# Optimization experiments

Measured on AMD Instinct MI355X. Metric: run time of the kernel, lower is better.

## Reference

```python
import jax, jax.numpy as jnp
import numpy as np

D_WIN = 6
SIGMA = D_WIN / 2.0  # sigma = D/2
EPS = 1e-6


def _ln(x, g, b):
    m = jnp.mean(x, -1, keepdims=True)
    v = jnp.var(x, -1, keepdims=True)
    return (x - m) / jnp.sqrt(v + EPS) * g + b


def _cross_attn(q, kv, Wq, Wkv, Wproj, bproj, nh):
    # standard multi-head cross attention, no qkv bias (qkv_bias=False)
    B, S, C = q.shape
    N = kv.shape[1]
    hd = C // nh
    scale = hd ** -0.5
    qh = (q @ Wq).reshape(B, S, nh, hd).transpose(0, 2, 1, 3) * scale
    kvh = (kv @ Wkv).reshape(B, N, 2, nh, hd).transpose(2, 0, 3, 1, 4)
    k, v = kvh[0], kvh[1]
    attn = jax.nn.softmax(jnp.einsum('bhsd,bhnd->bhsn', qh, k), -1)
    x = jnp.einsum('bhsn,bhnd->bhsd', attn, v).transpose(0, 2, 1, 3).reshape(B, S, C)
    return x @ Wproj + bproj


def setup_inputs() -> dict:
    key = jax.random.key(0)
    ks = jax.random.split(key, 32)
    B, S, C, H, W = 32, 128, 384, 8, 512

    def lin(k, i, o):
        return jax.random.normal(k, (i, o), jnp.float32) * 0.02

    inp = {
        'q': jax.random.normal(ks[0], (B, S, C), jnp.float32),
        'kv': jax.random.normal(ks[1], (B, H * W, C), jnp.float32),
        # main attention linears (qkv_bias=False)
        'Wq': lin(ks[2], C, C),
        'Wkv': lin(ks[3], C, 2 * C),
        'Wproj': lin(ks[4], C, C), 'bproj': jnp.zeros((C,), jnp.float32),
        # position predictor
        'Wp_w': lin(ks[5], C, C), 'Wp_b': jnp.zeros((C,), jnp.float32),
        'vp_w': lin(ks[6], C, 1), 'vp_b': jnp.zeros((1,), jnp.float32),
        'Wqpos': lin(ks[7], C, C), 'bqpos': jnp.zeros((C,), jnp.float32),
        # simplified RCTC decoder projection
        'Wrctc': lin(ks[8], C, C), 'brctc': jnp.zeros((C,), jnp.float32),
        # pt_to_question cross attention (2 heads)
        'ca1_Wq': lin(ks[9], C, C), 'ca1_Wkv': lin(ks[10], C, 2 * C),
        'ca1_Wproj': lin(ks[11], C, C), 'ca1_bproj': jnp.zeros((C,), jnp.float32),
        # pt_to_image cross attention (2 heads)
        'ca2_Wq': lin(ks[12], C, C), 'ca2_Wkv': lin(ks[13], C, 2 * C),
        'ca2_Wproj': lin(ks[14], C, C), 'ca2_bproj': jnp.zeros((C,), jnp.float32),
        # layernorms
        'g_q1': jnp.ones((C,), jnp.float32), 'b_q1': jnp.zeros((C,), jnp.float32),
        'g_kv1': jnp.ones((C,), jnp.float32), 'b_kv1': jnp.zeros((C,), jnp.float32),
        'g_q2': jnp.ones((C,), jnp.float32), 'b_q2': jnp.zeros((C,), jnp.float32),
        'g_kv2': jnp.ones((C,), jnp.float32), 'b_kv2': jnp.zeros((C,), jnp.float32),
        'sz_h': H, 'sz_w': W,
    }
    return inp


def reference(q, kv, Wq, Wkv, Wproj, bproj, Wp_w, Wp_b, vp_w, vp_b, Wqpos, bqpos,
              Wrctc, brctc, ca1_Wq, ca1_Wkv, ca1_Wproj, ca1_bproj,
              ca2_Wq, ca2_Wkv, ca2_Wproj, ca2_bproj,
              g_q1, b_q1, g_kv1, b_kv1, g_q2, b_q2, g_kv2, b_kv2, sz_h, sz_w):
    B, N, C = kv.shape
    S = q.shape[1]
    H, W = sz_h, sz_w
    nh = 1
    hd = C // nh
    scale = hd ** -0.5

    # RCTC decoder (simplified): (B,N,C) -> (B,C,H,W) -> collapse H -> (B,W,C) -> linear
    kv_img = kv.transpose(0, 2, 1).reshape(B, C, H, W)
    dec = kv_img.mean(axis=2).transpose(0, 2, 1)  # (B, W, C)
    dec = dec @ Wrctc + brctc

    qh = (q @ Wq).reshape(B, S, nh, hd).transpose(0, 2, 1, 3) * scale  # (B,nh,S,hd)
    kvh = (dec @ Wkv).reshape(B, W, 2, nh, hd).transpose(2, 0, 3, 1, 4)
    k, v = kvh[0], kvh[1]  # (B,nh,W,hd)

    # position prediction branch
    p = q @ Wqpos + bqpos
    p = _cross_attn(_ln(p, g_q1, b_q1), _ln(q, g_kv1, b_kv1),
                    ca1_Wq, ca1_Wkv, ca1_Wproj, ca1_bproj, 2)
    p = _cross_attn(_ln(p, g_q2, b_q2), _ln(dec, g_kv2, b_kv2),
                    ca2_Wq, ca2_Wkv, ca2_Wproj, ca2_bproj, 2)
    p_t = jax.nn.sigmoid(jnp.tanh(p @ Wp_w + Wp_b) @ vp_w + vp_b) * W  # (B,S,1)

    # Gaussian window mask around predicted position
    idx = jnp.arange(W, dtype=jnp.float32)[None, None, None, :]     # (1,1,1,W)
    pexp = p_t[:, None, :, :]                                        # (B,1,S,1)
    gauss = jnp.exp(-(idx - pexp) ** 2 / (2.0 * SIGMA ** 2))         # (B,1,S,W)

    attn = jnp.einsum('bhsd,bhwd->bhsw', qh, k) * gauss
    attn = jax.nn.softmax(attn, -1)
    x = jnp.einsum('bhsw,bhwd->bhsd', attn, v).transpose(0, 2, 1, 3).reshape(B, S, C)
    return x @ Wproj + bproj
```

## Files before the change

### kernel.cpp

```cpp
#include <hip/hip_runtime.h>
#include <hip/hip_bf16.h>
#include <math.h>

#define B_ 32
#define S_ 128
#define C_ 384
#define H_ 8
#define W_ 512
#define NKV 4096

typedef __attribute__((ext_vector_type(8))) short short8;
typedef __attribute__((ext_vector_type(4))) float floatx4;

static __device__ __forceinline__ ushort f2bf(float v) {
    __hip_bfloat16 h = __float2bfloat16(v);
    return *(ushort*)&h;
}
static __device__ __forceinline__ float ldf(const float* p, size_t i) { return p[i]; }
static __device__ __forceinline__ float ldf(const ushort* p, size_t i) {
    union { uint u; float f; } c; c.u = (uint)p[i] << 16; return c.f;
}

__global__ __launch_bounds__(256) void prep_kernel(const float* __restrict__ kv,
                                                   ushort* __restrict__ dec0b,
                                                   const float* __restrict__ q,
                                                   ushort* __restrict__ qb) {
    int v = blockIdx.x * 256 + threadIdx.x;
    const int meanTot = B_ * W_ * (C_ / 4);
    if (v < meanTot) {
        int c4  = v % (C_ / 4);
        int row = v / (C_ / 4);
        int b = row / W_;
        int w = row % W_;
        const float4* src = (const float4*)kv + (size_t)(b * NKV + w) * (C_ / 4) + c4;
        float4 s = {0.f, 0.f, 0.f, 0.f};
#pragma unroll
        for (int h = 0; h < H_; ++h) {
            float4 t = src[(size_t)h * W_ * (C_ / 4)];
            s.x += t.x; s.y += t.y; s.z += t.z; s.w += t.w;
        }
        ushort4 o;
        o.x = f2bf(s.x * 0.125f); o.y = f2bf(s.y * 0.125f);
        o.z = f2bf(s.z * 0.125f); o.w = f2bf(s.w * 0.125f);
        ((ushort4*)dec0b)[v] = o;
        return;
    }
    v -= meanTot;
    const int castTot = B_ * S_ * (C_ / 4);
    if (v >= castTot) return;
    float4 f = ((const float4*)q)[v];
    ushort4 o;
    o.x = f2bf(f.x); o.y = f2bf(f.y); o.z = f2bf(f.z); o.w = f2bf(f.w);
    ((ushort4*)qb)[v] = o;
}

struct WtDesc { const float* src[12]; ushort* dst[12]; int Kd[12]; int Nd[12]; };
__global__ __launch_bounds__(256) void wtcast_kernel(WtDesc d) {
    int wi = blockIdx.y;
    int K = d.Kd[wi], N = d.Nd[wi];
    int tiles_n = N / 32;
    int tile = blockIdx.x;
    if (tile >= (K / 32) * tiles_n) return;
    int k0 = (tile / tiles_n) * 32, n0 = (tile % tiles_n) * 32;
    __shared__ float t[32][33];
    int tid = threadIdx.x;
    int r = tid >> 3, c4 = (tid & 7) * 4;
    float4 v = *(const float4*)&d.src[wi][(size_t)(k0 + r) * N + n0 + c4];
    t[r][c4] = v.x; t[r][c4 + 1] = v.y; t[r][c4 + 2] = v.z; t[r][c4 + 3] = v.w;
    __syncthreads();
    int c = tid >> 3, k4 = (tid & 7) * 4;
    ushort4 o;
    o.x = f2bf(t[k4][c]); o.y = f2bf(t[k4 + 1][c]);
    o.z = f2bf(t[k4 + 2][c]); o.w = f2bf(t[k4 + 3][c]);
    *(ushort4*)&d.dst[wi][(size_t)(n0 + c) * K + k0 + k4] = o;
}

struct GJob {
    const ushort* A; const ushort* Bt;
    const float* bias; float* Cout; ushort* Cbf;
    int M, N, K; float alpha; int act;
};
struct GJobs { GJob j[3]; };

__global__ __launch_bounds__(256) void bgemm_kernel(GJobs gs) {
    const GJob g = gs.j[blockIdx.z];
    const int bm = blockIdx.y * 128, bn = blockIdx.x * 128;
    if (bm >= g.M || bn >= g.N) return;
    __shared__ ushort As[128 * 40];
    __shared__ ushort Bs[128 * 40];
    const int tid = threadIdx.x;
    const int wav = tid >> 6, lane = tid & 63;
    const int wm = (wav >> 1) * 64, wn = (wav & 1) * 64;
    const int lrow = lane & 15, lq = lane >> 4;

    floatx4 acc[4][4] = {};

    const int sr = tid >> 1, sc0 = (tid & 1) * 16;
    const ushort* Ag = g.A + (size_t)(bm + sr) * g.K + sc0;
    const ushort* Bg = g.Bt + (size_t)(bn + sr) * g.K + sc0;
    ushort* Asw = &As[sr * 40 + sc0];
    ushort* Bsw = &Bs[sr * 40 + sc0];

    uint4 a0 = *(const uint4*)(Ag);
    uint4 a1 = *(const uint4*)(Ag + 8);
    uint4 b0 = *(const uint4*)(Bg);
    uint4 b1 = *(const uint4*)(Bg + 8);

    for (int k0 = 0; k0 < g.K; k0 += 32) {
        __syncthreads();
        *(uint4*)Asw = a0; *(uint4*)(Asw + 8) = a1;
        *(uint4*)Bsw = b0; *(uint4*)(Bsw + 8) = b1;
        __syncthreads();
        if (k0 + 32 < g.K) {
            a0 = *(const uint4*)(Ag + k0 + 32);
            a1 = *(const uint4*)(Ag + k0 + 40);
            b0 = *(const uint4*)(Bg + k0 + 32);
            b1 = *(const uint4*)(Bg + k0 + 40);
        }
        short8 af[4], bfr[4];
#pragma unroll
        for (int i = 0; i < 4; ++i)
            af[i] = *(const short8*)&As[(wm + 16 * i + lrow) * 40 + lq * 8];
#pragma unroll
        for (int j = 0; j < 4; ++j)
            bfr[j] = *(const short8*)&Bs[(wn + 16 * j + lrow) * 40 + lq * 8];
#pragma unroll
        for (int i = 0; i < 4; ++i)
#pragma unroll
            for (int j = 0; j < 4; ++j)
                acc[i][j] = __builtin_amdgcn_mfma_f32_16x16x32_bf16(af[i], bfr[j], acc[i][j], 0, 0, 0);
    }

#pragma unroll
    for (int i = 0; i < 4; ++i)
#pragma unroll
        for (int j = 0; j < 4; ++j) {
            int row = bm + wm + 16 * i + lq * 4;
            int col = bn + wn + 16 * j + lrow;
            float bv = g.bias ? g.bias[col] : 0.f;
#pragma unroll
            for (int r = 0; r < 4; ++r) {
                float v = acc[i][j][r] * g.alpha + bv;
                if (g.act == 1) v = tanhf(v);
                size_t off = (size_t)(row + r) * g.N + col;
                if (g.Cout) g.Cout[off] = v;
                if (g.Cbf) g.Cbf[off] = f2bf(v);
            }
        }
}

static inline void bgemmJ(hipStream_t st, int nj, const GJob* js) {
    GJobs gs;
    int mx = 0, my = 0;
    for (int i = 0; i < nj; ++i) {
        gs.j[i] = js[i];
        int nx = js[i].N / 128, ny = js[i].M / 128;
        if (nx > mx) mx = nx;
        if (ny > my) my = ny;
    }
    for (int i = nj; i < 3; ++i) gs.j[i] = js[0];
    bgemm_kernel<<<dim3(mx, my, nj), 256, 0, st>>>(gs);
}

struct BGArgs {
    const ushort* A; const ushort* Bt;
    const float* bias; float* outF; ushort* outB;
    int lda, ldb, ldo;
    long AsB, BsB, OsB;
    int AsH, BsH, OsH;
    int K, NH;
    float alpha; int act;
    int nbat;
    const ushort* vtsrc; ushort* vtdst; int vtNw;
};
__global__ __launch_bounds__(256) void battn_kernel(BGArgs g) {
    __shared__ ushort As[64 * 40];
    __shared__ ushort Bs[64 * 40];
    const int tid = threadIdx.x;
    const int bat = blockIdx.z;
    if (bat >= g.nbat) {
        int flat = (bat - g.nbat) * (gridDim.x * gridDim.y)
                 + blockIdx.y * gridDim.x + blockIdx.x;
        int wt_n = g.vtNw >> 5;
        int tiles = wt_n * (C_ / 32);
        if (flat >= B_ * tiles) return;
        int b  = flat / tiles, rr = flat % tiles;
        int w0 = (rr % wt_n) * 32, c0 = (rr / wt_n) * 32;
        ushort (*t)[33] = (ushort (*)[33])As;
        int wl = tid >> 3, c4 = (tid & 7) * 4;
        ushort4 v = *(const ushort4*)&g.vtsrc[((size_t)b * g.vtNw + w0 + wl) * 768 + 384 + c0 + c4];
        t[wl][c4] = v.x; t[wl][c4 + 1] = v.y; t[wl][c4 + 2] = v.z; t[wl][c4 + 3] = v.w;
        __syncthreads();
        int dl = tid >> 3, w4 = (tid & 7) * 4;
        ushort4 o;
        o.x = t[w4][dl]; o.y = t[w4 + 1][dl]; o.z = t[w4 + 2][dl]; o.w = t[w4 + 3][dl];
        *(ushort4*)&g.vtdst[((size_t)b * C_ + c0 + dl) * g.vtNw + w0 + w4] = o;
        return;
    }
    const int bn = blockIdx.x * 64, bm = blockIdx.y * 64;
    const int bb = bat / g.NH, hh = bat % g.NH;
    const ushort* A  = g.A  + (size_t)bb * g.AsB + (size_t)hh * g.AsH;
    const ushort* Bt = g.Bt + (size_t)bb * g.BsB + (size_t)hh * g.BsH;
    const int wav = tid >> 6, lane = tid & 63;
    const int lrow = lane & 15, lq = lane >> 4;
    const int sr = tid >> 2, sc0 = (tid & 3) * 8;
    const ushort* Ag = A  + (size_t)(bm + sr) * g.lda + sc0;
    const ushort* Bg = Bt + (size_t)(bn + sr) * g.ldb + sc0;
    ushort* Asw = &As[sr * 40 + sc0];
    ushort* Bsw = &Bs[sr * 40 + sc0];

    floatx4 acc[4] = {};

    uint4 a = *(const uint4*)(Ag);
    uint4 b = *(const uint4*)(Bg);

    for (int k0 = 0; k0 < g.K; k0 += 32) {
        __syncthreads();
        *(uint4*)Asw = a; *(uint4*)Bsw = b;
        __syncthreads();
        if (k0 + 32 < g.K) {
            a = *(const uint4*)(Ag + k0 + 32);
            b = *(const uint4*)(Bg + k0 + 32);
        }
        short8 af = *(const short8*)&As[(wav * 16 + lrow) * 40 + lq * 8];
#pragma unroll
        for (int j = 0; j < 4; ++j) {
            short8 bf = *(const short8*)&Bs[(16 * j + lrow) * 40 + lq * 8];
            acc[j] = __builtin_amdgcn_mfma_f32_16x16x32_bf16(af, bf, acc[j], 0, 0, 0);
        }
    }

#pragma unroll
    for (int j = 0; j < 4; ++j) {
        int col = bn + 16 * j + lrow;
        float bv = g.bias ? g.bias[col] : 0.f;
        int row0 = bm + wav * 16 + lq * 4;
#pragma unroll
        for (int r = 0; r < 4; ++r) {
            float v = acc[j][r] * g.alpha + bv;
            if (g.act == 1) v = tanhf(v);
            size_t off = (size_t)bb * g.OsB + (size_t)hh * g.OsH
                       + (size_t)(row0 + r) * g.ldo + col;
            if (g.outF) g.outF[off] = v;
            if (g.outB) g.outB[off] = f2bf(v);
        }
    }
}

static inline void battn(hipStream_t st, const ushort* A, const ushort* Bt,
                         const float* bias, float* outF, ushort* outB,
                         int M, int N, int K, float alpha, int act,
                         int lda, long AsB, int AsH,
                         int ldb, long BsB, int BsH,
                         int ldo, long OsB, int OsH,
                         int NH, int nbat,
                         const ushort* vtsrc = nullptr, ushort* vtdst = nullptr,
                         int vtNw = 0) {
    BGArgs g;
    g.A = A; g.Bt = Bt; g.bias = bias; g.outF = outF; g.outB = outB;
    g.lda = lda; g.ldb = ldb; g.ldo = ldo;
    g.AsB = AsB; g.BsB = BsB; g.OsB = OsB;
    g.AsH = AsH; g.BsH = BsH; g.OsH = OsH;
    g.K = K; g.NH = NH; g.alpha = alpha; g.act = act;
    g.nbat = nbat; g.vtsrc = vtsrc; g.vtdst = vtdst; g.vtNw = vtNw;
    int gx = N / 64, gy = M / 64, gz = nbat;
    if (vtsrc) {
        int nvt = B_ * (vtNw / 32) * (C_ / 32);
        int per = gx * gy;
        gz += (nvt + per - 1) / per;
    }
    battn_kernel<<<dim3(gx, gy, gz), 256, 0, st>>>(g);
}

static inline void bgemm64(hipStream_t st, const ushort* A, const ushort* Bt,
                           const float* bias, float* outF, ushort* outB,
                           int M, int N, int K, float alpha, int act) {
    battn(st, A, Bt, bias, outF, outB, M, N, K, alpha, act,
          K, 0, 0, K, 0, 0, N, 0, 0, 1, 1);
}

struct Ln2Desc {
    const void* X0; const float* g0; const float* b0; ushort* Y0; int bf0; int rows0;
    const void* X1; const float* g1; const float* b1; ushort* Y1; int bf1;
};
__global__ __launch_bounds__(128) void ln2_kernel(Ln2Desc d) {
    int row = blockIdx.x;
    const void* X; const float* g; const float* bb; ushort* Y; int isbf;
    if (row < d.rows0) { X = d.X0; g = d.g0; bb = d.b0; Y = d.Y0; isbf = d.bf0; }
    else { row -= d.rows0; X = d.X1; g = d.g1; bb = d.b1; Y = d.Y1; isbf = d.bf1; }
    const float*  xf = (const float*)X + (size_t)row * C_;
    const ushort* xb = (const ushort*)X + (size_t)row * C_;
    ushort* y = Y + (size_t)row * C_;
    int t = threadIdx.x;
    float v0, v1, v2;
    if (isbf) { v0 = ldf(xb, t); v1 = ldf(xb, t + 128); v2 = ldf(xb, t + 256); }
    else      { v0 = ldf(xf, t); v1 = ldf(xf, t + 128); v2 = ldf(xf, t + 256); }
    float s = v0 + v1 + v2, sq = v0 * v0 + v1 * v1 + v2 * v2;
    __shared__ float rs[128], rq[128];
    rs[t] = s; rq[t] = sq; __syncthreads();
    if (t < 64) {
        s = rs[t] + rs[t + 64]; sq = rq[t] + rq[t + 64];
        for (int o = 32; o; o >>= 1) { s += __shfl_down(s, o); sq += __shfl_down(sq, o); }
        if (t == 0) { rs[0] = s; rq[0] = sq; }
    }
    __syncthreads();
    float mean = rs[0] * (1.0f / C_);
    float var  = rq[0] * (1.0f / C_) - mean * mean;
    float inv  = rsqrtf(var + 1e-6f);
    y[t]       = f2bf((v0 - mean) * inv * g[t]       + bb[t]);
    y[t + 128] = f2bf((v1 - mean) * inv * g[t + 128] + bb[t + 128]);
    y[t + 256] = f2bf((v2 - mean) * inv * g[t + 256] + bb[t + 256]);
}

template <int NW, int GAUSS>
__global__ __launch_bounds__(256) void softmax_kernel(
    const float* __restrict__ sc, const float* __restrict__ ptv,
    ushort* __restrict__ P)
{
    int row = blockIdx.x * 4 + (threadIdx.x >> 6);
    int lane = threadIdx.x & 63;
    const float* s = sc + (size_t)row * NW;
    float pcen = GAUSS ? ptv[row] : 0.f;
    float vals[NW / 64];
    float m = -1e30f;
#pragma unroll
    for (int i = 0; i < NW / 64; ++i) {
        int w = lane + 64 * i;
        float v = s[w];
        if (GAUSS) { float dw = (float)w - pcen; v *= expf(dw * dw * (-1.0f / 18.0f)); }
        vals[i] = v; m = fmaxf(m, v);
    }
#pragma unroll
    for (int o = 32; o; o >>= 1) m = fmaxf(m, __shfl_xor(m, o));
    float sum = 0.f;
#pragma unroll
    for (int i = 0; i < NW / 64; ++i) { vals[i] = expf(vals[i] - m); sum += vals[i]; }
#pragma unroll
    for (int o = 32; o; o >>= 1) sum += __shfl_xor(sum, o);
    float rinv = 1.0f / sum;
    ushort* op = P + (size_t)row * NW;
#pragma unroll
    for (int i = 0; i < NW / 64; ++i) op[lane + 64 * i] = f2bf(vals[i] * rinv);
}

__global__ __launch_bounds__(128) void pt_kernel(const float* __restrict__ T,
    const float* __restrict__ vpw, const float* __restrict__ vpb,
    float* __restrict__ out) {
    int row = blockIdx.x;
    int t = threadIdx.x;
    const float* x = T + (size_t)row * C_;
    float s = x[t] * vpw[t] + x[t + 128] * vpw[t + 128] + x[t + 256] * vpw[t + 256];
    __shared__ float red[128];
    red[t] = s; __syncthreads();
    if (t < 64) {
        s = red[t] + red[t + 64];
        for (int o = 32; o; o >>= 1) s += __shfl_down(s, o);
        if (t == 0) {
            float z = s + vpb[0];
            out[row] = 512.0f / (1.0f + expf(-z));
        }
    }
}

extern "C" void kernel_launch(void* const* d_in, const int* in_sizes, int n_in,
                              void* d_out, int out_size, void* d_ws, size_t ws_size,
                              hipStream_t stream) {
    const float* q     = (const float*)d_in[0];
    const float* kv    = (const float*)d_in[1];
    const float* Wq    = (const float*)d_in[2];
    const float* Wkv   = (const float*)d_in[3];
    const float* Wproj = (const float*)d_in[4];
    const float* bproj = (const float*)d_in[5];
    const float* Wp_w  = (const float*)d_in[6];
    const float* Wp_b  = (const float*)d_in[7];
    const float* vp_w  = (const float*)d_in[8];
    const float* vp_b  = (const float*)d_in[9];
    const float* Wqpos = (const float*)d_in[10];
    const float* bqpos = (const float*)d_in[11];
    const float* Wrctc = (const float*)d_in[12];
    const float* brctc = (const float*)d_in[13];
    const float* ca1_Wq    = (const float*)d_in[14];
    const float* ca1_Wkv   = (const float*)d_in[15];
    const float* ca1_Wproj = (const float*)d_in[16];
    const float* ca1_bproj = (const float*)d_in[17];
    const float* ca2_Wq    = (const float*)d_in[18];
    const float* ca2_Wkv   = (const float*)d_in[19];
    const float* ca2_Wproj = (const float*)d_in[20];
    const float* ca2_bproj = (const float*)d_in[21];
    const float* g_q1  = (const float*)d_in[22];
    const float* b_q1  = (const float*)d_in[23];
    const float* g_kv1 = (const float*)d_in[24];
    const float* b_kv1 = (const float*)d_in[25];
    const float* g_q2  = (const float*)d_in[26];
    const float* b_q2  = (const float*)d_in[27];
    const float* g_kv2 = (const float*)d_in[28];
    const float* b_kv2 = (const float*)d_in[29];
    float* out = (float*)d_out;
    float* ws  = (float*)d_ws;

    ushort* dec0b = (ushort*)(ws);
    ushort* wb    = (ushort*)(ws + 3145728);
    ushort* qb    = (ushort*)(ws + 4251648);
    ushort* decb  = (ushort*)(ws + 5038080);
    ushort* qhb   = (ushort*)(ws + 8183808);
    float*  p     = ws + 8970240;
    ushort* pb    = (ushort*)(ws + 10543104);
    float*  t1    = ws + 11329536;
    ushort* t1b   = (ushort*)(ws + 12902400);
    ushort* t2b   = (ushort*)(ws + 13688832);
    ushort* qpb   = (ushort*)(ws + 16834560);
    ushort* kvb   = (ushort*)(ws + 17620992);
    ushort* vt    = (ushort*)(ws + 23912448);
    float*  sc    = ws + 27058176;
    ushort* Pb    = (ushort*)(ws + 31252480);
    ushort* xb    = (ushort*)(ws + 33349632);
    float*  ptb   = ws + 34136064;

    ushort* wbWq     = wb;
    ushort* wbWqpos  = wb + 147456;
    ushort* wbWrctc  = wb + 294912;
    ushort* wbC1Wq   = wb + 442368;
    ushort* wbC1Wp   = wb + 589824;
    ushort* wbC2Wq   = wb + 737280;
    ushort* wbC2Wp   = wb + 884736;
    ushort* wbWpw    = wb + 1032192;
    ushort* wbWproj  = wb + 1179648;
    ushort* wbWkv    = wb + 1327104;
    ushort* wbC1Wkv  = wb + 1622016;
    ushort* wbC2Wkv  = wb + 1916928;

    const float rs384 = 0.05103103630798288f;
    const float rs192 = 0.07216878364870323f;

    prep_kernel<<<(B_ * W_ * (C_ / 4) + B_ * S_ * (C_ / 4) + 255) / 256, 256, 0, stream>>>(
        kv, dec0b, q, qb);
    {
        WtDesc d;
        const float* s_[12] = {Wq, Wqpos, Wrctc, ca1_Wq, ca1_Wproj, ca2_Wq, ca2_Wproj,
                               Wp_w, Wproj, Wkv, ca1_Wkv, ca2_Wkv};
        ushort* t_[12] = {wbWq, wbWqpos, wbWrctc, wbC1Wq, wbC1Wp, wbC2Wq, wbC2Wp,
                          wbWpw, wbWproj, wbWkv, wbC1Wkv, wbC2Wkv};
        for (int i = 0; i < 12; ++i) {
            d.src[i] = s_[i]; d.dst[i] = t_[i];
            d.Kd[i] = 384; d.Nd[i] = (i >= 9) ? 768 : 384;
        }
        dim3 grid(288, 12);
        wtcast_kernel<<<grid, 256, 0, stream>>>(d);
    }
    {
        GJob js[3];
        js[0] = {dec0b, wbWrctc, brctc, nullptr, decb, B_ * W_, 384, 384, 1.f, 0};
        js[1] = {qb, wbWq, nullptr, nullptr, qhb, B_ * S_, 384, 384, rs384, 0};
        js[2] = {qb, wbWqpos, bqpos, p, nullptr, B_ * S_, 384, 384, 1.f, 0};
        bgemmJ(stream, 3, js);
    }
    {
        Ln2Desc d;
        d.X0 = p; d.g0 = g_q1;  d.b0 = b_q1;  d.Y0 = t1b; d.bf0 = 0; d.rows0 = B_ * S_;
        d.X1 = q; d.g1 = g_kv1; d.b1 = b_kv1; d.Y1 = t2b; d.bf1 = 0;
        ln2_kernel<<<2 * B_ * S_, 128, 0, stream>>>(d);
    }
    {
        GJob js[2];
        js[0] = {t1b, wbC1Wq, nullptr, nullptr, qpb, B_ * S_, 384, 384, rs192, 0};
        js[1] = {t2b, wbC1Wkv, nullptr, nullptr, kvb, B_ * S_, 768, 384, 1.f, 0};
        bgemmJ(stream, 2, js);
    }
    battn(stream, qpb, kvb, nullptr, sc, nullptr, 128, 128, 192, 1.f, 0,
          384, (long)S_ * 384, 192,
          768, (long)S_ * 768, 192,
          128, (long)2 * S_ * 128, S_ * 128, 2, 64,
          kvb, vt, S_);
    softmax_kernel<128, 0><<<(B_ * 2 * S_) / 4, 256, 0, stream>>>(sc, nullptr, Pb);
    battn(stream, Pb, vt, nullptr, nullptr, xb, 128, 192, 128, 1.f, 0,
          128, (long)2 * S_ * 128, S_ * 128,
          128, (long)C_ * S_, 192 * S_,
          384, (long)S_ * 384, 192, 2, 64);
    bgemm64(stream, xb, wbC1Wp, ca1_bproj, p, nullptr, B_ * S_, 384, 384, 1.f, 0);
    {
        Ln2Desc d;
        d.X0 = p;    d.g0 = g_q2;  d.b0 = b_q2;  d.Y0 = t1b; d.bf0 = 0; d.rows0 = B_ * S_;
        d.X1 = decb; d.g1 = g_kv2; d.b1 = b_kv2; d.Y1 = t2b; d.bf1 = 1;
        ln2_kernel<<<B_ * S_ + B_ * W_, 128, 0, stream>>>(d);
    }
    {
        GJob js[2];
        js[0] = {t1b, wbC2Wq, nullptr, nullptr, qpb, B_ * S_, 384, 384, rs192, 0};
        js[1] = {t2b, wbC2Wkv, nullptr, nullptr, kvb, B_ * W_, 768, 384, 1.f, 0};
        bgemmJ(stream, 2, js);
    }
    battn(stream, qpb, kvb, nullptr, sc, nullptr, 128, 512, 192, 1.f, 0,
          384, (long)S_ * 384, 192,
          768, (long)W_ * 768, 192,
          512, (long)2 * S_ * 512, S_ * 512, 2, 64,
          kvb, vt, W_);
    softmax_kernel<512, 0><<<(B_ * 2 * S_) / 4, 256, 0, stream>>>(sc, nullptr, Pb);
    battn(stream, Pb, vt, nullptr, nullptr, xb, 128, 192, 512, 1.f, 0,
          512, (long)2 * S_ * 512, S_ * 512,
          512, (long)C_ * W_, 192 * W_,
          384, (long)S_ * 384, 192, 2, 64);
    bgemm64(stream, xb, wbC2Wp, ca2_bproj, p, pb, B_ * S_, 384, 384, 1.f, 0);
    {
        GJob js[2];
        js[0] = {pb, wbWpw, Wp_b, t1, nullptr, B_ * S_, 384, 384, 1.f, 1};
        js[1] = {decb, wbWkv, nullptr, nullptr, kvb, B_ * W_, 768, 384, 1.f, 0};
        bgemmJ(stream, 2, js);
    }
    pt_kernel<<<B_ * S_, 128, 0, stream>>>(t1, vp_w, vp_b, ptb);
    battn(stream, qhb, kvb, nullptr, sc, nullptr, 128, 512, 384, 1.f, 0,
          384, (long)S_ * 384, 0,
          768, (long)W_ * 768, 0,
          512, (long)S_ * 512, 0, 1, 32,
          kvb, vt, W_);
    softmax_kernel<512, 1><<<(B_ * S_) / 4, 256, 0, stream>>>(sc, ptb, Pb);
    battn(stream, Pb, vt, nullptr, nullptr, xb, 128, 384, 512, 1.f, 0,
          512, (long)S_ * 512, 0,
          512, (long)C_ * W_, 0,
          384, (long)S_ * 384, 0, 1, 32);
    bgemm64(stream, xb, wbWproj, bproj, out, nullptr, B_ * S_, 384, 384, 1.f, 0);
}
```

Measured before the change: 562.4 us.

## Fuse softmax into PV matmul and merge prep/weight-cast kernels

Replaces the separate softmax kernels and the following P·V batched GEMMs with one kernel. It computes each row's max and sum from the fp32 scores, then rebuilds the bf16 probabilities tile by tile while doing the MFMA product, scaling by the reciprocal sum at the end. This removes the bf16 P round-trip through global memory and three kernel launches. The input prep and weight-cast kernels are also merged into one launch. In exchange, each output-column block recomputes the row statistics and exponentials, which reads the score matrix several times and adds redundant expf work.

```diff
diff --git a/kernel.cpp b/kernel.cpp
--- a/kernel.cpp
+++ b/kernel.cpp
@@ -21,58 +21,58 @@
     union { uint u; float f; } c; c.u = (uint)p[i] << 16; return c.f;
 }
 
-__global__ __launch_bounds__(256) void prep_kernel(const float* __restrict__ kv,
-                                                   ushort* __restrict__ dec0b,
-                                                   const float* __restrict__ q,
-                                                   ushort* __restrict__ qb) {
-    int v = blockIdx.x * 256 + threadIdx.x;
-    const int meanTot = B_ * W_ * (C_ / 4);
-    if (v < meanTot) {
+struct PrepDesc {
+    const float* kv; ushort* dec0b; const float* q; ushort* qb;
+    const float* wsrc[12]; ushort* wdst[12]; int wN[12];
+};
+__global__ __launch_bounds__(256) void prep2_kernel(PrepDesc d) {
+    __shared__ float t[32][33];
+    const int meanB = B_ * W_ * (C_ / 4) / 256;
+    const int castB = B_ * S_ * (C_ / 4) / 256;
+    int bid = blockIdx.x;
+    int tid = threadIdx.x;
+    if (bid < meanB) {
+        int v = bid * 256 + tid;
         int c4  = v % (C_ / 4);
         int row = v / (C_ / 4);
         int b = row / W_;
         int w = row % W_;
-        const float4* src = (const float4*)kv + (size_t)(b * NKV + w) * (C_ / 4) + c4;
+        const float4* src = (const float4*)d.kv + (size_t)(b * NKV + w) * (C_ / 4) + c4;
         float4 s = {0.f, 0.f, 0.f, 0.f};
 #pragma unroll
         for (int h = 0; h < H_; ++h) {
-            float4 t = src[(size_t)h * W_ * (C_ / 4)];
-            s.x += t.x; s.y += t.y; s.z += t.z; s.w += t.w;
+            float4 x = src[(size_t)h * W_ * (C_ / 4)];
+            s.x += x.x; s.y += x.y; s.z += x.z; s.w += x.w;
         }
         ushort4 o;
         o.x = f2bf(s.x * 0.125f); o.y = f2bf(s.y * 0.125f);
         o.z = f2bf(s.z * 0.125f); o.w = f2bf(s.w * 0.125f);
-        ((ushort4*)dec0b)[v] = o;
+        ((ushort4*)d.dec0b)[v] = o;
         return;
     }
-    v -= meanTot;
-    const int castTot = B_ * S_ * (C_ / 4);
-    if (v >= castTot) return;
-    float4 f = ((const float4*)q)[v];
-    ushort4 o;
-    o.x = f2bf(f.x); o.y = f2bf(f.y); o.z = f2bf(f.z); o.w = f2bf(f.w);
-    ((ushort4*)qb)[v] = o;
-}
-
-struct WtDesc { const float* src[12]; ushort* dst[12]; int Kd[12]; int Nd[12]; };
-__global__ __launch_bounds__(256) void wtcast_kernel(WtDesc d) {
-    int wi = blockIdx.y;
-    int K = d.Kd[wi], N = d.Nd[wi];
+    if (bid < meanB + castB) {
+        int v = (bid - meanB) * 256 + tid;
+        float4 f = ((const float4*)d.q)[v];
+        ushort4 o;
+        o.x = f2bf(f.x); o.y = f2bf(f.y); o.z = f2bf(f.z); o.w = f2bf(f.w);
+        ((ushort4*)d.qb)[v] = o;
+        return;
+    }
+    int f = bid - meanB - castB;
+    int wi = f / 288, tile = f % 288;
+    int N = d.wN[wi];
     int tiles_n = N / 32;
-    int tile = blockIdx.x;
-    if (tile >= (K / 32) * tiles_n) return;
+    if (tile >= 12 * tiles_n) return;
     int k0 = (tile / tiles_n) * 32, n0 = (tile % tiles_n) * 32;
-    __shared__ float t[32][33];
-    int tid = threadIdx.x;
     int r = tid >> 3, c4 = (tid & 7) * 4;
-    float4 v = *(const float4*)&d.src[wi][(size_t)(k0 + r) * N + n0 + c4];
+    float4 v = *(const float4*)&d.wsrc[wi][(size_t)(k0 + r) * N + n0 + c4];
     t[r][c4] = v.x; t[r][c4 + 1] = v.y; t[r][c4 + 2] = v.z; t[r][c4 + 3] = v.w;
     __syncthreads();
     int c = tid >> 3, k4 = (tid & 7) * 4;
     ushort4 o;
     o.x = f2bf(t[k4][c]); o.y = f2bf(t[k4 + 1][c]);
     o.z = f2bf(t[k4 + 2][c]); o.w = f2bf(t[k4 + 3][c]);
-    *(ushort4*)&d.dst[wi][(size_t)(n0 + c) * K + k0 + k4] = o;
+    *(ushort4*)&d.wdst[wi][(size_t)(n0 + c) * 384 + k0 + k4] = o;
 }
 
 struct GJob {
@@ -279,6 +279,103 @@
           K, 0, 0, K, 0, 0, N, 0, 0, 1, 1);
 }
 
+struct PVArgs {
+    const float* sc; const float* ptv; const ushort* Bt; ushort* outB;
+    int ldb, ldo; long BsB, OsB; int BsH, OsH; int NH;
+};
+template <int NW, int GAUSS>
+__global__ __launch_bounds__(256) void pvsm_kernel(PVArgs g) {
+    __shared__ ushort As[64 * 40];
+    __shared__ ushort Bs[64 * 40];
+    __shared__ float msh[64], rsh[64];
+    const int bn = blockIdx.x * 64, bm = blockIdx.y * 64;
+    const int bat = blockIdx.z, bb = bat / g.NH, hh = bat % g.NH;
+    const int tid = threadIdx.x;
+    const int wav = tid >> 6, lane = tid & 63;
+    const int lrow = lane & 15, lq = lane >> 4;
+    const float* Sg = g.sc + (size_t)bat * S_ * NW + (size_t)bm * NW;
+
+    for (int rr = wav * 16; rr < wav * 16 + 16; ++rr) {
+        float pcen = 0.f;
+        if (GAUSS) pcen = g.ptv[(size_t)bat * S_ + bm + rr];
+        float v[NW / 64];
+        float m = -1e30f;
+#pragma unroll
+        for (int i = 0; i < NW / 64; ++i) {
+            int w = lane + 64 * i;
+            float x = Sg[(size_t)rr * NW + w];
+            if (GAUSS) { float dw = (float)w - pcen; x *= expf(dw * dw * (-1.0f / 18.0f)); }
+            v[i] = x; m = fmaxf(m, x);
+        }
+#pragma unroll
+        for (int o = 32; o; o >>= 1) m = fmaxf(m, __shfl_xor(m, o));
+        float s = 0.f;
+#pragma unroll
+        for (int i = 0; i < NW / 64; ++i) s += expf(v[i] - m);
+#pragma unroll
+        for (int o = 32; o; o >>= 1) s += __shfl_xor(s, o);
+        if (lane == 0) { msh[rr] = m; rsh[rr] = 1.0f / s; }
+    }
+    __syncthreads();
+
+    const int sr = tid >> 2, sc0 = (tid & 3) * 8;
+    const ushort* Bg = g.Bt + (size_t)bb * g.BsB + (size_t)hh * g.BsH
+                     + (size_t)(bn + sr) * g.ldb + sc0;
+    ushort* Asw = &As[sr * 40 + sc0];
+    ushort* Bsw = &Bs[sr * 40 + sc0];
+    const float mrow = msh[sr];
+    float pcen_s = 0.f;
+    if (GAUSS) pcen_s = g.ptv[(size_t)bat * S_ + bm + sr];
+    const float* Ssr = Sg + (size_t)sr * NW;
+
+    floatx4 acc[4] = {};
+    float4 f0 = *(const float4*)(Ssr + sc0);
+    float4 f1 = *(const float4*)(Ssr + sc0 + 4);
+    uint4 b = *(const uint4*)(Bg);
+
+    for (int k0 = 0; k0 < NW; k0 += 32) {
+        float xv[8] = {f0.x, f0.y, f0.z, f0.w, f1.x, f1.y, f1.z, f1.w};
+        ushort av[8] __attribute__((aligned(16)));
+#pragma unroll
+        for (int j = 0; j < 8; ++j) {
+            float x = xv[j];
+            if (GAUSS) {
+                float dw = (float)(k0 + sc0 + j) - pcen_s;
+                x *= expf(dw * dw * (-1.0f / 18.0f));
+            }
+            av[j] = f2bf(expf(x - mrow));
+        }
+        __syncthreads();
+        *(uint4*)Asw = *(const uint4*)av;
+        *(uint4*)Bsw = b;
+        __syncthreads();
+        if (k0 + 32 < NW) {
+            f0 = *(const float4*)(Ssr + k0 + 32 + sc0);
+            f1 = *(const float4*)(Ssr + k0 + 36 + sc0);
+            b  = *(const uint4*)(Bg + k0 + 32);
+        }
+        short8 af = *(const short8*)&As[(wav * 16 + lrow) * 40 + lq * 8];
+#pragma unroll
+        for (int j = 0; j < 4; ++j) {
+            short8 bf = *(const short8*)&Bs[(16 * j + lrow) * 40 + lq * 8];
+            acc[j] = __builtin_amdgcn_mfma_f32_16x16x32_bf16(af, bf, acc[j], 0, 0, 0);
+        }
+    }
+
+#pragma unroll
+    for (int j = 0; j < 4; ++j) {
+        int col = bn + 16 * j + lrow;
+        int lr0 = wav * 16 + lq * 4;
+#pragma unroll
+        for (int r = 0; r < 4; ++r) {
+            float v = acc[j][r] * rsh[lr0 + r];
+            size_t off = (size_t)bb * g.OsB + (size_t)hh * g.OsH
+                       + (size_t)(bm + lr0 + r) * g.ldo + col;
+            g.outB[off] = f2bf(v);
+        }
+    }
+}
+
 struct Ln2Desc {
     const void* X0; const float* g0; const float* b0; ushort* Y0; int bf0; int rows0;
     const void* X1; const float* g1; const float* b1; ushort* Y1; int bf1;
@@ -310,37 +407,6 @@
     y[t]       = f2bf((v0 - mean) * inv * g[t]       + bb[t]);
     y[t + 128] = f2bf((v1 - mean) * inv * g[t + 128] + bb[t + 128]);
     y[t + 256] = f2bf((v2 - mean) * inv * g[t + 256] + bb[t + 256]);
-}
-
-template <int NW, int GAUSS>
-__global__ __launch_bounds__(256) void softmax_kernel(
-    const float* __restrict__ sc, const float* __restrict__ ptv,
-    ushort* __restrict__ P)
-{
-    int row = blockIdx.x * 4 + (threadIdx.x >> 6);
-    int lane = threadIdx.x & 63;
-    const float* s = sc + (size_t)row * NW;
-    float pcen = GAUSS ? ptv[row] : 0.f;
-    float vals[NW / 64];
-    float m = -1e30f;
-#pragma unroll
-    for (int i = 0; i < NW / 64; ++i) {
-        int w = lane + 64 * i;
-        float v = s[w];
-        if (GAUSS) { float dw = (float)w - pcen; v *= expf(dw * dw * (-1.0f / 18.0f)); }
-        vals[i] = v; m = fmaxf(m, v);
-    }
-#pragma unroll
-    for (int o = 32; o; o >>= 1) m = fmaxf(m, __shfl_xor(m, o));
-    float sum = 0.f;
-#pragma unroll
-    for (int i = 0; i < NW / 64; ++i) { vals[i] = expf(vals[i] - m); sum += vals[i]; }
-#pragma unroll
-    for (int o = 32; o; o >>= 1) sum += __shfl_xor(sum, o);
-    float rinv = 1.0f / sum;
-    ushort* op = P + (size_t)row * NW;
-#pragma unroll
-    for (int i = 0; i < NW / 64; ++i) op[lane + 64 * i] = f2bf(vals[i] * rinv);
 }
 
 __global__ __launch_bounds__(128) void pt_kernel(const float* __restrict__ T,
@@ -412,7 +478,6 @@
     ushort* kvb   = (ushort*)(ws + 17620992);
     ushort* vt    = (ushort*)(ws + 23912448);
     float*  sc    = ws + 27058176;
-    ushort* Pb    = (ushort*)(ws + 31252480);
     ushort* xb    = (ushort*)(ws + 33349632);
     float*  ptb   = ws + 34136064;
 
@@ -432,20 +497,18 @@
     const float rs384 = 0.05103103630798288f;
     const float rs192 = 0.07216878364870323f;
 
-    prep_kernel<<<(B_ * W_ * (C_ / 4) + B_ * S_ * (C_ / 4) + 255) / 256, 256, 0, stream>>>(
-        kv, dec0b, q, qb);
-    {
-        WtDesc d;
+    {
+        PrepDesc d;
+        d.kv = kv; d.dec0b = dec0b; d.q = q; d.qb = qb;
         const float* s_[12] = {Wq, Wqpos, Wrctc, ca1_Wq, ca1_Wproj, ca2_Wq, ca2_Wproj,
                                Wp_w, Wproj, Wkv, ca1_Wkv, ca2_Wkv};
         ushort* t_[12] = {wbWq, wbWqpos, wbWrctc, wbC1Wq, wbC1Wp, wbC2Wq, wbC2Wp,
                           wbWpw, wbWproj, wbWkv, wbC1Wkv, wbC2Wkv};
         for (int i = 0; i < 12; ++i) {
-            d.src[i] = s_[i]; d.dst[i] = t_[i];
-            d.Kd[i] = 384; d.Nd[i] = (i >= 9) ? 768 : 384;
-        }
-        dim3 grid(288, 12);
-        wtcast_kernel<<<grid, 256, 0, stream>>>(d);
+            d.wsrc[i] = s_[i]; d.wdst[i] = t_[i];
+            d.wN[i] = (i >= 9) ? 768 : 384;
+        }
+        prep2_kernel<<<6144 + 1536 + 3456, 256, 0, stream>>>(d);
     }
     {
         GJob js[3];
@@ -471,11 +534,14 @@
           768, (long)S_ * 768, 192,
           128, (long)2 * S_ * 128, S_ * 128, 2, 64,
           kvb, vt, S_);
-    softmax_kernel<128, 0><<<(B_ * 2 * S_) / 4, 256, 0, stream>>>(sc, nullptr, Pb);
-    battn(stream, Pb, vt, nullptr, nullptr, xb, 128, 192, 128, 1.f, 0,
-          128, (long)2 * S_ * 128, S_ * 128,
-          128, (long)C_ * S_, 192 * S_,
-          384, (long)S_ * 384, 192, 2, 64);
+    {
+        PVArgs a;
+        a.sc = sc; a.ptv = nullptr; a.Bt = vt; a.outB = xb;
+        a.ldb = S_; a.ldo = 384;
+        a.BsB = (long)C_ * S_; a.BsH = 192 * S_;
+        a.OsB = (long)S_ * 384; a.OsH = 192; a.NH = 2;
+        pvsm_kernel<128, 0><<<dim3(3, 2, 64), 256, 0, stream>>>(a);
+    }
     bgemm64(stream, xb, wbC1Wp, ca1_bproj, p, nullptr, B_ * S_, 384, 384, 1.f, 0);
     {
         Ln2Desc d;
@@ -494,11 +560,14 @@
           768, (long)W_ * 768, 192,
           512, (long)2 * S_ * 512, S_ * 512, 2, 64,
           kvb, vt, W_);
-    softmax_kernel<512, 0><<<(B_ * 2 * S_) / 4, 256, 0, stream>>>(sc, nullptr, Pb);
-    battn(stream, Pb, vt, nullptr, nullptr, xb, 128, 192, 512, 1.f, 0,
-          512, (long)2 * S_ * 512, S_ * 512,
-          512, (long)C_ * W_, 192 * W_,
-          384, (long)S_ * 384, 192, 2, 64);
+    {
+        PVArgs a;
+        a.sc = sc; a.ptv = nullptr; a.Bt = vt; a.outB = xb;
+        a.ldb = W_; a.ldo = 384;
+        a.BsB = (long)C_ * W_; a.BsH = 192 * W_;
+        a.OsB = (long)S_ * 384; a.OsH = 192; a.NH = 2;
+        pvsm_kernel<512, 0><<<dim3(3, 2, 64), 256, 0, stream>>>(a);
+    }
     bgemm64(stream, xb, wbC2Wp, ca2_bproj, p, pb, B_ * S_, 384, 384, 1.f, 0);
     {
         GJob js[2];
@@ -512,10 +581,13 @@
           768, (long)W_ * 768, 0,
           512, (long)S_ * 512, 0, 1, 32,
           kvb, vt, W_);
-    softmax_kernel<512, 1><<<(B_ * S_) / 4, 256, 0, stream>>>(sc, ptb, Pb);
-    battn(stream, Pb, vt, nullptr, nullptr, xb, 128, 384, 512, 1.f, 0,
-          512, (long)S_ * 512, 0,
-          512, (long)C_ * W_, 0,
-          384, (long)S_ * 384, 0, 1, 32);
+    {
+        PVArgs a;
+        a.sc = sc; a.ptv = ptb; a.Bt = vt; a.outB = xb;
+        a.ldb = W_; a.ldo = 384;
+        a.BsB = (long)C_ * W_; a.BsH = 0;
+        a.OsB = (long)S_ * 384; a.OsH = 0; a.NH = 1;
+        pvsm_kernel<512, 1><<<dim3(6, 2, 32), 256, 0, stream>>>(a);
+    }
     bgemm64(stream, xb, wbWproj, bproj, out, nullptr, B_ * S_, 384, 384, 1.f, 0);
 }
```

After: 612.8 us. 9.0% more time.
